# Optimization experiments

Hardware: AMD Instinct MI355X
Metric: run time of the kernel (lower is better)

## Reference

```python
import jax, jax.numpy as jnp
import numpy as np

D_MODEL = 1024
NHEAD = 8
HEAD_DIM = D_MODEL // NHEAD
D_FF = 4096
EPS_ATTN = 1e-6
EPS_LN = 1e-5


def _layernorm(x, g, b):
    mu = jnp.mean(x, axis=-1, keepdims=True)
    var = jnp.var(x, axis=-1, keepdims=True)
    return (x - mu) * jax.lax.rsqrt(var + EPS_LN) * g + b


def _linear_attention(q, k, v):
    # q,k,v: [N, L, H, D]
    Q = jax.nn.elu(q) + 1.0
    K = jax.nn.elu(k) + 1.0
    v_length = v.shape[1]
    v = v / v_length
    KV = jnp.einsum('nshd,nshv->nhdv', K, v)           # [N,H,D,D]
    Z = 1.0 / (jnp.einsum('nlhd,nhd->nlh', Q, K.sum(axis=1)) + EPS_ATTN)
    out = jnp.einsum('nlhd,nhdv,nlh->nlhv', Q, KV, Z) * v_length
    return out


def setup_inputs() -> dict:
    key = jax.random.key(0)
    ks = jax.random.split(key, 12)
    s = 1.0 / np.sqrt(D_MODEL)
    sf = 1.0 / np.sqrt(D_FF)
    return {
        'x': jax.random.normal(ks[0], (2, 4096, D_MODEL), jnp.float32),
        'wq': jax.random.normal(ks[1], (D_MODEL, D_MODEL), jnp.float32) * s,
        'wk': jax.random.normal(ks[2], (D_MODEL, D_MODEL), jnp.float32) * s,
        'wv': jax.random.normal(ks[3], (D_MODEL, D_MODEL), jnp.float32) * s,
        'w1': jax.random.normal(ks[4], (D_FF, D_MODEL), jnp.float32) * s,
        'b1': jnp.zeros((D_FF,), jnp.float32),
        'w2': jax.random.normal(ks[5], (D_MODEL, D_FF), jnp.float32) * sf,
        'b2': jnp.zeros((D_MODEL,), jnp.float32),
        'g1': jnp.ones((D_MODEL,), jnp.float32),
        'be1': jnp.zeros((D_MODEL,), jnp.float32),
        'g2': jnp.ones((D_MODEL,), jnp.float32),
        'be2': jnp.zeros((D_MODEL,), jnp.float32),
    }


def reference(x, wq, wk, wv, w1, b1, w2, b2, g1, be1, g2, be2):
    N, L, C = x.shape
    # pre-norm self attention
    x2 = _layernorm(x, g1, be1)
    q = (x2 @ wq.T).reshape(N, L, NHEAD, HEAD_DIM)
    k = (x2 @ wk.T).reshape(N, L, NHEAD, HEAD_DIM)
    v = (x2 @ wv.T).reshape(N, L, NHEAD, HEAD_DIM)
    msg = _linear_attention(q, k, v).reshape(N, L, C)
    x = x + msg
    # MLP block
    x2 = _layernorm(x, g2, be2)
    h = jax.nn.gelu(x2 @ w1.T + b1, approximate=False)
    x = x + (h @ w2.T + b2)
    return x
```

## Files before the change

### kernel.cpp

```cpp
#include <hip/hip_runtime.h>
#include <hip/hip_bf16.h>
#include <math.h>

typedef __bf16 bf16x8 __attribute__((ext_vector_type(8)));
typedef __bf16 bf16x4 __attribute__((ext_vector_type(4)));
typedef float f32x4 __attribute__((ext_vector_type(4)));

#define DEVI __device__ __forceinline__

DEVI void gload_lds16(const __bf16* g, __bf16* l) {
    __builtin_amdgcn_global_load_lds(
        (const __attribute__((address_space(1))) unsigned int*)g,
        (__attribute__((address_space(3))) unsigned int*)l, 16, 0, 0);
}

DEVI float fast_erf(float x) {
    const float ax = __builtin_fabsf(x);
    const float t = __builtin_amdgcn_rcpf(__builtin_fmaf(0.3275911f, ax, 1.0f));
    float p = __builtin_fmaf(1.061405429f, t, -1.453152027f);
    p = __builtin_fmaf(p, t, 1.421413741f);
    p = __builtin_fmaf(p, t, -0.284496736f);
    p = __builtin_fmaf(p, t, 0.254829592f);
    const float e = __expf(-ax * ax);
    const float r = __builtin_fmaf(-p * t, e, 1.0f);
    return __builtin_copysignf(r, x);
}

DEVI float gelu_exact(float v) {
    return 0.5f * v * (1.0f + fast_erf(v * 0.70710678118654752f));
}

DEVI int swz128(int row, int col) { return row * 128 + (col ^ ((row & 7) << 3)); }

__global__ void sniff_kernel(const unsigned short* __restrict__ x, int* flags) {
    const int tid = threadIdx.x;
    const unsigned short u = x[tid * 2];
    const int e = (u >> 7) & 0xFF;
    const int zero = (u == 0) ? 1 : 0;
    const int sane = ((e >= 0x71 && e <= 0x8E) || ((u & 0x7FFF) == 0)) ? 1 : 0;
    const unsigned long long mz = __ballot(zero != 0);
    const unsigned long long ms = __ballot(sane != 0);
    __shared__ int wz[4], wsn[4];
    if ((tid & 63) == 0) { wz[tid >> 6] = __popcll(mz); wsn[tid >> 6] = __popcll(ms); }
    __syncthreads();
    if (tid == 0) {
        const int nz = wz[0] + wz[1] + wz[2] + wz[3];
        const int ns = wsn[0] + wsn[1] + wsn[2] + wsn[3];
        flags[0] = (nz >= 192 || ns < 128) ? 1 : 0;
    }
}

DEVI void conv8(const void* src, __bf16* dst, int si, int di, int isf32) {
    if (isf32) {
        const float* s = (const float*)src + si;
        bf16x8 o;
#pragma unroll
        for (int j = 0; j < 8; j++) o[j] = (__bf16)s[j];
        *(bf16x8*)(dst + di) = o;
    } else {
        *(uint4*)(dst + di) = *(const uint4*)((const __bf16*)src + si);
    }
}

__global__ __launch_bounds__(256) void convert_kernel(const void* __restrict__ src,
                                                      __bf16* __restrict__ dst, int n,
                                                      const int* __restrict__ flags) {
    const int i = (blockIdx.x * 256 + threadIdx.x) * 8;
    if (i >= n) return;
    conv8(src, dst, i, i, flags[0]);
}

__global__ __launch_bounds__(256) void convert3_kernel(const void* s0, const void* s1,
                                                       const void* s2, __bf16* __restrict__ dst,
                                                       const int* __restrict__ flags) {
    const int i = (blockIdx.x * 256 + threadIdx.x) * 8;
    const int which = i >> 20;
    const int off = i & 1048575;
    const void* s = (which == 0) ? s0 : ((which == 1) ? s1 : s2);
    conv8(s, dst, off, i, flags[0]);
}

struct Ptr6 { const void* p[6]; };
__global__ __launch_bounds__(256) void convert_small(Ptr6 srcs, __bf16* __restrict__ d0,
                                                     __bf16* __restrict__ d1,
                                                     const int* __restrict__ flags) {
    const int idx = (blockIdx.x * 256 + threadIdx.x) * 8;
    if (idx >= 9216) return;
    const int f = flags[0];
    if (idx < 4096) {
        conv8(srcs.p[0], d0, idx, idx, f);
    } else {
        const int j = idx - 4096;
        conv8(srcs.p[1 + (j >> 10)], d1, j & 1023, j, f);
    }
}

__global__ __launch_bounds__(256) void convert_ln_kernel(
    const void* __restrict__ src, const __bf16* __restrict__ g,
    const __bf16* __restrict__ b, __bf16* __restrict__ cx,
    __bf16* __restrict__ x2, const int* __restrict__ flags) {
    const size_t row = blockIdx.x;
    const int tid = threadIdx.x;
    float v[4];
    if (flags[0]) {
        const float4 f = *((const float4*)((const float*)src + row * 1024) + tid);
        v[0] = f.x; v[1] = f.y; v[2] = f.z; v[3] = f.w;
    } else {
        const bf16x4 f = *((const bf16x4*)((const __bf16*)src + row * 1024) + tid);
#pragma unroll
        for (int i = 0; i < 4; i++) v[i] = (float)f[i];
    }
    bf16x4 o;
#pragma unroll
    for (int i = 0; i < 4; i++) o[i] = (__bf16)v[i];
    *((bf16x4*)(cx + row * 1024) + tid) = o;

    float s = v[0] + v[1] + v[2] + v[3];
    float s2 = v[0] * v[0] + v[1] * v[1] + v[2] * v[2] + v[3] * v[3];
#pragma unroll
    for (int m = 32; m >= 1; m >>= 1) {
        s += __shfl_xor(s, m, 64);
        s2 += __shfl_xor(s2, m, 64);
    }
    __shared__ float rs[4], rs2[4];
    const int wave = tid >> 6, lane = tid & 63;
    if (lane == 0) { rs[wave] = s; rs2[wave] = s2; }
    __syncthreads();
    s = rs[0] + rs[1] + rs[2] + rs[3];
    s2 = rs2[0] + rs2[1] + rs2[2] + rs2[3];
    const float mu = s * (1.0f / 1024.0f);
    const float var = s2 * (1.0f / 1024.0f) - mu * mu;
    const float inv = rsqrtf(var + 1e-5f);
#pragma unroll
    for (int i = 0; i < 4; i++) {
        const int c = tid * 4 + i;
        x2[row * 1024 + c] = (__bf16)((v[i] - mu) * inv * (float)g[c] + (float)b[c]);
    }
}

template <typename T>
__global__ __launch_bounds__(256) void ln_kernel(const T* __restrict__ x,
                                                 const __bf16* __restrict__ g,
                                                 const __bf16* __restrict__ b,
                                                 __bf16* __restrict__ out) {
    const size_t row = blockIdx.x;
    const T* xr = x + row * 1024;
    const int tid = threadIdx.x;
    float v[4];
#pragma unroll
    for (int i = 0; i < 4; i++) v[i] = (float)xr[tid * 4 + i];
    float s = v[0] + v[1] + v[2] + v[3];
    float s2 = v[0] * v[0] + v[1] * v[1] + v[2] * v[2] + v[3] * v[3];
#pragma unroll
    for (int m = 32; m >= 1; m >>= 1) {
        s += __shfl_xor(s, m, 64);
        s2 += __shfl_xor(s2, m, 64);
    }
    __shared__ float rs[4], rs2[4];
    const int wave = tid >> 6, lane = tid & 63;
    if (lane == 0) { rs[wave] = s; rs2[wave] = s2; }
    __syncthreads();
    s = rs[0] + rs[1] + rs[2] + rs[3];
    s2 = rs2[0] + rs2[1] + rs2[2] + rs2[3];
    const float mu = s * (1.0f / 1024.0f);
    const float var = s2 * (1.0f / 1024.0f) - mu * mu;
    const float inv = rsqrtf(var + 1e-5f);
#pragma unroll
    for (int i = 0; i < 4; i++) {
        const int c = tid * 4 + i;
        out[row * 1024 + c] = (__bf16)((v[i] - mu) * inv * (float)g[c] + (float)b[c]);
    }
}

enum { EP_NONE = 0, EP_ELU1 = 1, EP_BIAS_GELU = 2, EP_BIAS_RES = 3, EP_QKV = 4 };

template <int EP, typename OutT>
__global__ __launch_bounds__(256, 4) void gemm_bt(
    const __bf16* __restrict__ A, const __bf16* __restrict__ B,
    const __bf16* __restrict__ bias, const float* resid,
    OutT* C, int M, int N, int K) {
    const int nwg = gridDim.x * gridDim.y;
    int bid = blockIdx.y * gridDim.x + blockIdx.x;
    bid = (bid & 7) * (nwg >> 3) + (bid >> 3);
    const int bm = bid / gridDim.x, bn = bid % gridDim.x;

    const int tid = threadIdx.x;
    const int wave = tid >> 6, lane = tid & 63;
    const int wm = wave & 1, wn = wave >> 1;
    const int lm = lane & 15, lq = lane >> 4;

    __shared__ __align__(16) __bf16 Asmem[2][128 * 32];
    __shared__ __align__(16) __bf16 Bsmem[2][128 * 32];

    f32x4 acc[4][4] = {};

    const __bf16* Abase = A + (size_t)bm * 128 * K;
    const __bf16* Bbase = B + (size_t)bn * 128 * K;

    const int sr = tid >> 2;
    const int sc = (((tid & 3) ^ ((tid >> 3) & 3))) << 3;
    const int wb = wave * 512;

    const __bf16* Ap0 = Abase + (size_t)sr * K + sc;
    const __bf16* Ap1 = Abase + (size_t)(sr + 64) * K + sc;
    const __bf16* Bp0 = Bbase + (size_t)sr * K + sc;
    const __bf16* Bp1 = Bbase + (size_t)(sr + 64) * K + sc;

    const int rg = ((lq ^ ((lm >> 1) & 3))) << 3;

#define STAGE(b, kk)                              \
    do {                                          \
        gload_lds16(Ap0 + (kk), &Asmem[b][wb]);   \
        gload_lds16(Ap1 + (kk), &Asmem[b][2048 + wb]); \
        gload_lds16(Bp0 + (kk), &Bsmem[b][wb]);   \
        gload_lds16(Bp1 + (kk), &Bsmem[b][2048 + wb]); \
    } while (0)

    STAGE(0, 0);
    __syncthreads();
    int cur = 0;
    for (int k0 = 0; k0 < K; k0 += 32) {
        if (k0 + 32 < K) STAGE(cur ^ 1, k0 + 32);
        bf16x8 af[4], bfv[4];
#pragma unroll
        for (int i = 0; i < 4; i++) {
            af[i]  = *(const bf16x8*)&Asmem[cur][(wm * 64 + i * 16 + lm) * 32 + rg];
            bfv[i] = *(const bf16x8*)&Bsmem[cur][(wn * 64 + i * 16 + lm) * 32 + rg];
        }
#pragma unroll
        for (int i = 0; i < 4; i++)
#pragma unroll
            for (int j = 0; j < 4; j++)
                acc[i][j] = __builtin_amdgcn_mfma_f32_16x16x32_bf16(af[i], bfv[j], acc[i][j], 0, 0, 0);
        __syncthreads();
        cur ^= 1;
    }
#undef STAGE

    const int row0 = bm * 128 + wm * 64;
    const int col0 = bn * 128 + wn * 64;
#pragma unroll
    for (int i = 0; i < 4; i++) {
#pragma unroll
        for (int j = 0; j < 4; j++) {
            const int col = col0 + j * 16 + lm;
#pragma unroll
            for (int r = 0; r < 4; r++) {
                const int row = row0 + i * 16 + lq * 4 + r;
                float v = acc[i][j][r];
                if (EP == EP_QKV) {
                    const int which = col >> 10;
                    if (which < 2) v = (v > 0.0f) ? (v + 1.0f) : __expf(v);
                    ((__bf16*)C)[(size_t)which * 8388608 + (size_t)row * 1024 + (col & 1023)] = (__bf16)v;
                    continue;
                }
                if (EP == EP_ELU1) {
                    v = (v > 0.0f) ? (v + 1.0f) : __expf(v);
                } else if (EP == EP_BIAS_GELU) {
                    v += (float)bias[col];
                    v = gelu_exact(v);
                } else if (EP == EP_BIAS_RES) {
                    v += (float)bias[col];
                    v += resid[(size_t)row * N + col];
                }
                C[(size_t)row * N + col] = (OutT)v;
            }
        }
    }
}

__global__ __launch_bounds__(256, 2) void gemm_bt_k64(
    const __bf16* __restrict__ A, const __bf16* __restrict__ B,
    const __bf16* __restrict__ bias, const float* resid,
    float* C, int M, int N, int K) {
    const int nwg = gridDim.x * gridDim.y;
    int bid = blockIdx.y * gridDim.x + blockIdx.x;
    bid = (bid & 7) * (nwg >> 3) + (bid >> 3);
    const int bm = bid / gridDim.x, bn = bid % gridDim.x;

    const int tid = threadIdx.x;
    const int wave = tid >> 6, lane = tid & 63;
    const int wm = wave & 1, wn = wave >> 1;
    const int lm = lane & 15, lq = lane >> 4;

    __shared__ __align__(16) __bf16 Asmem[2][128 * 64];
    __shared__ __align__(16) __bf16 Bsmem[2][128 * 64];

    f32x4 acc[4][4] = {};

    const __bf16* Abase = A + (size_t)bm * 128 * K;
    const __bf16* Bbase = B + (size_t)bn * 128 * K;

    const int sr = tid >> 3;
    const int sc = (((tid & 7) ^ ((tid >> 3) & 7))) << 3;
    const int wb = wave * 512;

    const __bf16* Ap[4];
    const __bf16* Bp[4];
#pragma unroll
    for (int p = 0; p < 4; p++) {
        Ap[p] = Abase + (size_t)(p * 32 + sr) * K + sc;
        Bp[p] = Bbase + (size_t)(p * 32 + sr) * K + sc;
    }

#define STAGE64(b, kk)                                        \
    do {                                                      \
        _Pragma("unroll")                                     \
        for (int p = 0; p < 4; p++) {                         \
            gload_lds16(Ap[p] + (kk), &Asmem[b][p * 2048 + wb]); \
            gload_lds16(Bp[p] + (kk), &Bsmem[b][p * 2048 + wb]); \
        }                                                     \
    } while (0)

    STAGE64(0, 0);
    __syncthreads();
    int cur = 0;
    for (int k0 = 0; k0 < K; k0 += 64) {
        if (k0 + 64 < K) STAGE64(cur ^ 1, k0 + 64);
        bf16x8 af[2][4], bfv[2][4];
#pragma unroll
        for (int h = 0; h < 2; h++) {
            const int rg = ((h * 4 + lq) ^ (lm & 7)) << 3;
#pragma unroll
            for (int i = 0; i < 4; i++) {
                af[h][i]  = *(const bf16x8*)&Asmem[cur][(wm * 64 + i * 16 + lm) * 64 + rg];
                bfv[h][i] = *(const bf16x8*)&Bsmem[cur][(wn * 64 + i * 16 + lm) * 64 + rg];
            }
        }
#pragma unroll
        for (int h = 0; h < 2; h++)
#pragma unroll
            for (int i = 0; i < 4; i++)
#pragma unroll
                for (int j = 0; j < 4; j++)
                    acc[i][j] = __builtin_amdgcn_mfma_f32_16x16x32_bf16(af[h][i], bfv[h][j], acc[i][j], 0, 0, 0);
        __syncthreads();
        cur ^= 1;
    }
#undef STAGE64

    const int row0 = bm * 128 + wm * 64;
    const int col0 = bn * 128 + wn * 64;
#pragma unroll
    for (int i = 0; i < 4; i++) {
#pragma unroll
        for (int j = 0; j < 4; j++) {
            const int col = col0 + j * 16 + lm;
            const float bcol = (float)bias[col];
#pragma unroll
            for (int r = 0; r < 4; r++) {
                const int row = row0 + i * 16 + lq * 4 + r;
                float v = acc[i][j][r] + bcol;
                v += resid[(size_t)row * N + col];
                C[(size_t)row * N + col] = v;
            }
        }
    }
}

__global__ __launch_bounds__(256) void kv_kernel(const __bf16* __restrict__ Kf,
                                                 const __bf16* __restrict__ Vf,
                                                 float* __restrict__ pkv,
                                                 float* __restrict__ pks) {
    const int nh = blockIdx.x, sc = blockIdx.y, vh = blockIdx.z;
    const int n = nh >> 3, h = nh & 7;
    const int tid = threadIdx.x;
    const int tv = tid & 15, td = tid >> 4;
    __shared__ __align__(16) __bf16 Kt[32 * 128];
    __shared__ __align__(16) __bf16 Vt[32 * 64];
    float acc[8][4] = {};
    float ks[8] = {};
    const size_t rowbase = (size_t)n * 4096 + (size_t)sc * 256;
    for (int s0 = 0; s0 < 256; s0 += 32) {
#pragma unroll
        for (int rep = 0; rep < 2; rep++) {
            const int s = tid + rep * 256;
            const int r = s >> 4, cs = (s & 15) * 8;
            const size_t gidx = (rowbase + s0 + r) * 1024 + h * 128 + cs;
            *(bf16x8*)&Kt[r * 128 + cs] = *(const bf16x8*)&Kf[gidx];
        }
        {
            const int r = tid >> 3, cs = (tid & 7) * 8;
            const size_t gidx = (rowbase + s0 + r) * 1024 + h * 128 + vh * 64 + cs;
            *(bf16x8*)&Vt[r * 64 + cs] = *(const bf16x8*)&Vf[gidx];
        }
        __syncthreads();
#pragma unroll 4
        for (int s = 0; s < 32; s++) {
            const bf16x8 k8 = *(const bf16x8*)&Kt[s * 128 + td * 8];
            const bf16x4 v4 = *(const bf16x4*)&Vt[s * 64 + tv * 4];
            float kk[8], vv[4];
#pragma unroll
            for (int i = 0; i < 8; i++) kk[i] = (float)k8[i];
#pragma unroll
            for (int j = 0; j < 4; j++) vv[j] = (float)v4[j];
#pragma unroll
            for (int i = 0; i < 8; i++) {
                ks[i] += kk[i];
#pragma unroll
                for (int j = 0; j < 4; j++) acc[i][j] += kk[i] * vv[j];
            }
        }
        __syncthreads();
    }
    float* dst = pkv + ((size_t)sc * 16 + nh) * 16384;
#pragma unroll
    for (int j = 0; j < 4; j++)
#pragma unroll
        for (int i = 0; i < 8; i++)
            dst[(vh * 64 + tv * 4 + j) * 128 + td * 8 + i] = acc[i][j];
    if (vh == 0 && tv == 0) {
        float* ds2 = pks + ((size_t)sc * 16 + nh) * 128;
#pragma unroll
        for (int i = 0; i < 8; i++) ds2[td * 8 + i] = ks[i];
    }
}

__global__ __launch_bounds__(256) void kv_reduce(const float* __restrict__ pkv,
                                                 const float* __restrict__ pks,
                                                 __bf16* __restrict__ kvbT,
                                                 float* __restrict__ ksf) {
    const int idx = blockIdx.x * 256 + threadIdx.x;
    float s = 0.0f;
#pragma unroll
    for (int c = 0; c < 16; c++) s += pkv[(size_t)c * 262144 + idx];
    kvbT[idx] = (__bf16)s;
    if (idx < 2048) {
        float t = 0.0f;
#pragma unroll
        for (int c = 0; c < 16; c++) t += pks[c * 2048 + idx];
        ksf[idx] = t;
    }
}

__global__ __launch_bounds__(256) void z_kernel(const __bf16* __restrict__ Qf,
                                                const float* __restrict__ ksf,
                                                float* __restrict__ zbuf) {
    const int idx = blockIdx.x * 256 + threadIdx.x;
    const int h = idx & 7;
    const size_t row = (size_t)(idx >> 3);
    const __bf16* q = Qf + row * 1024 + h * 128;
    const float* ks = ksf + ((size_t)((row >> 12) * 8 + h)) * 128;
    float s = 0.0f;
    for (int d = 0; d < 128; d += 8) {
        const bf16x8 q8 = *(const bf16x8*)&q[d];
#pragma unroll
        for (int j = 0; j < 8; j++) s += (float)q8[j] * ks[d + j];
    }
    zbuf[idx] = 1.0f / (s + 1e-6f);
}

__global__ __launch_bounds__(256, 3) void attn_out_kernel(
    const __bf16* __restrict__ x, const __bf16* __restrict__ Qf,
    const __bf16* __restrict__ kvbT, const float* __restrict__ zbuf,
    float* __restrict__ xmid) {
    const int nh = blockIdx.x, lc = blockIdx.y;
    const int n = nh >> 3, h = nh & 7;
    const int tid = threadIdx.x;
    const int wv = tid >> 6, lane = tid & 63;
    const int lm = lane & 15, lq = lane >> 4;
    __shared__ __align__(16) __bf16 KVs[128 * 128];
    __shared__ __align__(16) __bf16 Qs[64 * 128];
    __shared__ float Zs[64];
    const __bf16* kv = kvbT + (size_t)nh * 16384;
#pragma unroll
    for (int rep = 0; rep < 8; rep++) {
        const int i = tid + rep * 256;
        const int r = i >> 4, c8 = (i & 15) * 8;
        *(bf16x8*)&KVs[swz128(r, c8)] = *(const bf16x8*)&kv[i * 8];
    }
    const size_t gr0 = (size_t)n * 4096 + (size_t)lc * 64;
#pragma unroll
    for (int rep = 0; rep < 4; rep++) {
        const int s = tid + rep * 256;
        const int r = s >> 4, cs = (s & 15) * 8;
        *(bf16x8*)&Qs[swz128(r, cs)] =
            *(const bf16x8*)&Qf[(gr0 + r) * 1024 + h * 128 + cs];
    }
    if (tid < 64) Zs[tid] = zbuf[(gr0 + tid) * 8 + h];
    __syncthreads();

    const int xmask = (lm & 7) << 3;
    f32x4 acc[4][2] = {};
#pragma unroll
    for (int k0 = 0; k0 < 128; k0 += 32) {
        const int kk = (k0 + lq * 8) ^ xmask;
        bf16x8 af[4], bv[2];
#pragma unroll
        for (int i = 0; i < 4; i++)
            af[i] = *(const bf16x8*)&Qs[(i * 16 + lm) * 128 + kk];
#pragma unroll
        for (int j = 0; j < 2; j++)
            bv[j] = *(const bf16x8*)&KVs[(wv * 32 + j * 16 + lm) * 128 + kk];
#pragma unroll
        for (int i = 0; i < 4; i++)
#pragma unroll
            for (int j = 0; j < 2; j++)
                acc[i][j] = __builtin_amdgcn_mfma_f32_16x16x32_bf16(af[i], bv[j], acc[i][j], 0, 0, 0);
    }
#pragma unroll
    for (int i = 0; i < 4; i++) {
#pragma unroll
        for (int j = 0; j < 2; j++) {
            const int col = wv * 32 + j * 16 + lm;
#pragma unroll
            for (int r = 0; r < 4; r++) {
                const int lr = i * 16 + lq * 4 + r;
                const size_t gi = (gr0 + lr) * 1024 + h * 128 + col;
                xmid[gi] = (float)x[gi] + acc[i][j][r] * Zs[lr];
            }
        }
    }
}

extern "C" void kernel_launch(void* const* d_in, const int* in_sizes, int n_in,
                              void* d_out, int out_size, void* d_ws, size_t ws_size,
                              hipStream_t stream) {
    float* out = (float*)d_out;
    char* ws = (char*)d_ws;

    const int nx = 8388608, nw = 1048576, nw1 = 4194304, nb1 = 4096, ng = 1024;
    size_t off = 0;
    __bf16* cx   = (__bf16*)(ws + off); off += (size_t)nx * 2;
    __bf16* cwq  = (__bf16*)(ws + off); off += (size_t)nw * 2;
    __bf16* cwk  = (__bf16*)(ws + off); off += (size_t)nw * 2;
    __bf16* cwv  = (__bf16*)(ws + off); off += (size_t)nw * 2;
    __bf16* cw1  = (__bf16*)(ws + off); off += (size_t)nw1 * 2;
    __bf16* cb1  = (__bf16*)(ws + off); off += (size_t)nb1 * 2;
    __bf16* cw2  = (__bf16*)(ws + off); off += (size_t)nw1 * 2;
    __bf16* cb2  = (__bf16*)(ws + off); off += (size_t)ng * 2;
    __bf16* cg1  = (__bf16*)(ws + off); off += (size_t)ng * 2;
    __bf16* cbe1 = (__bf16*)(ws + off); off += (size_t)ng * 2;
    __bf16* cg2  = (__bf16*)(ws + off); off += (size_t)ng * 2;
    __bf16* cbe2 = (__bf16*)(ws + off); off += (size_t)ng * 2;
    int* flags = (int*)(ws + off); off += 64;
    (void)cwk; (void)cwv; (void)cg1; (void)cbe1; (void)cg2; (void)cbe2;

    char* PB = ws + off;
    __bf16* x2   = (__bf16*)(PB);
    __bf16* Qf   = (__bf16*)(PB + 16777216);
    __bf16* Kf   = (__bf16*)(PB + 33554432);
    __bf16* Vf   = (__bf16*)(PB + 50331648);
    float*  pkv  = (float*)(PB + 67108864);
    float*  pks  = (float*)(PB + 83886080);
    float*  ksf  = (float*)(PB + 84017152);
    float*  zbuf = (float*)(PB + 84025344);
    __bf16* kvbT = (__bf16*)(PB + 84287488);
    __bf16* hbuf = (__bf16*)(PB + 16777216);
    float*  xmid = out;

    sniff_kernel<<<1, 256, 0, stream>>>((const unsigned short*)d_in[0], flags);
    convert3_kernel<<<3 * nw / 2048, 256, 0, stream>>>(d_in[1], d_in[2], d_in[3], cwq, flags);
    convert_kernel<<<nw1 / 2048, 256, 0, stream>>>(d_in[4], cw1, nw1, flags);
    convert_kernel<<<nw1 / 2048, 256, 0, stream>>>(d_in[6], cw2, nw1, flags);
    Ptr6 sp;
    sp.p[0] = d_in[5];  sp.p[1] = d_in[7];  sp.p[2] = d_in[8];
    sp.p[3] = d_in[9];  sp.p[4] = d_in[10]; sp.p[5] = d_in[11];
    convert_small<<<5, 256, 0, stream>>>(sp, cb1, cb2, flags);

    convert_ln_kernel<<<8192, 256, 0, stream>>>(d_in[0], cg1, cbe1, cx, x2, flags);
    gemm_bt<EP_QKV, __bf16><<<dim3(3072 / 128, 8192 / 128), 256, 0, stream>>>(
        x2, cwq, nullptr, nullptr, Qf, 8192, 3072, 1024);
    kv_kernel<<<dim3(16, 16, 2), 256, 0, stream>>>(Kf, Vf, pkv, pks);
    kv_reduce<<<1024, 256, 0, stream>>>(pkv, pks, kvbT, ksf);
    z_kernel<<<256, 256, 0, stream>>>(Qf, ksf, zbuf);
    attn_out_kernel<<<dim3(16, 64), 256, 0, stream>>>(cx, Qf, kvbT, zbuf, xmid);
    ln_kernel<float><<<8192, 256, 0, stream>>>(xmid, cg2, cbe2, x2);
    gemm_bt<EP_BIAS_GELU, __bf16><<<dim3(4096 / 128, 8192 / 128), 256, 0, stream>>>(
        x2, cw1, cb1, nullptr, hbuf, 8192, 4096, 1024);
    gemm_bt_k64<<<dim3(1024 / 128, 8192 / 128), 256, 0, stream>>>(
        hbuf, cw2, cb2, xmid, out, 8192, 1024, 4096);
}
```

Baseline: 463.1 us.

## Use 256x256-tile 512-thread GEMM kernel for the FFN up-projection with GELU

Adds a dedicated GEMM kernel for the first MLP projection that uses 256x256 output tiles, 8 waves, and a double-buffered LDS pipeline fed by direct global-to-LDS loads, with bias plus exact GELU in the epilogue. The larger tile raises arithmetic intensity and halves the number of global loads per FLOP compared with the 128x128 kernel. In exchange it uses 128 KB of LDS and a large accumulator array, which may limit occupancy to one block per CU despite launch_bounds(512,2). The grid shrinks to 512 workgroups, which can hurt wave-quantization balance across CUs.

```diff
diff --git a/kernel.cpp b/kernel.cpp
--- a/kernel.cpp
+++ b/kernel.cpp
@@ -269,6 +269,106 @@
     }
 }
 
+__global__ __launch_bounds__(512, 2) void gemm256_gelu(
+    const __bf16* __restrict__ A, const __bf16* __restrict__ B,
+    const __bf16* __restrict__ bias, __bf16* __restrict__ C,
+    int M, int N, int K) {
+    const int nwg = gridDim.x * gridDim.y;
+    int bid = blockIdx.y * gridDim.x + blockIdx.x;
+    bid = (bid & 7) * (nwg >> 3) + (bid >> 3);
+    const int bm = bid / gridDim.x, bn = bid % gridDim.x;
+
+    const int tid = threadIdx.x;
+    const int wave = tid >> 6, lane = tid & 63;
+    const int wm = wave >> 2, wn = wave & 3;
+    const int lm = lane & 15, lq = lane >> 4;
+
+    __shared__ __align__(16) __bf16 Asmem[2][256 * 64];
+    __shared__ __align__(16) __bf16 Bsmem[2][256 * 64];
+
+    f32x4 acc[8][4] = {};
+
+    const int sr = tid >> 3;
+    const int sc = (((tid & 7) ^ ((tid >> 3) & 7))) << 3;
+    const int wdst = wave * 512;
+
+    const __bf16* Ap[4];
+    const __bf16* Bp[4];
+#pragma unroll
+    for (int p = 0; p < 4; p++) {
+        Ap[p] = A + (size_t)(bm * 256 + p * 64 + sr) * K + sc;
+        Bp[p] = B + (size_t)(bn * 256 + p * 64 + sr) * K + sc;
+    }
+
+#define STAGE256(b, kk)                                          \
+    do {                                                         \
+        _Pragma("unroll")                                        \
+        for (int p = 0; p < 4; p++) {                            \
+            gload_lds16(Ap[p] + (kk), &Asmem[b][p * 4096 + wdst]); \
+            gload_lds16(Bp[p] + (kk), &Bsmem[b][p * 4096 + wdst]); \
+        }                                                        \
+    } while (0)
+
+    STAGE256(0, 0);
+    STAGE256(1, 64);
+    asm volatile("s_waitcnt vmcnt(8)" ::: "memory");
+    __builtin_amdgcn_s_barrier();
+    asm volatile("" ::: "memory");
+
+    const int gsw = lm & 7;
+    const int nt = K >> 6;
+    int cur = 0;
+    for (int t = 0; t < nt; ++t) {
+#pragma unroll
+        for (int ks = 0; ks < 2; ks++) {
+            const int rg = ((ks * 4 + lq) ^ gsw) << 3;
+            bf16x8 af[8], bv[4];
+#pragma unroll
+            for (int i = 0; i < 8; i++)
+                af[i] = *(const bf16x8*)&Asmem[cur][(wm * 128 + i * 16 + lm) * 64 + rg];
+#pragma unroll
+            for (int j = 0; j < 4; j++)
+                bv[j] = *(const bf16x8*)&Bsmem[cur][(wn * 64 + j * 16 + lm) * 64 + rg];
+            __builtin_amdgcn_s_setprio(1);
+#pragma unroll
+            for (int i = 0; i < 8; i++)
+#pragma unroll
+                for (int j = 0; j < 4; j++)
+                    acc[i][j] = __builtin_amdgcn_mfma_f32_16x16x32_bf16(af[i], bv[j], acc[i][j], 0, 0, 0);
+            __builtin_amdgcn_s_setprio(0);
+        }
+        asm volatile("" ::: "memory");
+        __builtin_amdgcn_s_barrier();
+        asm volatile("" ::: "memory");
+        if (t + 2 < nt) {
+            STAGE256(cur, (t + 2) << 6);
+            asm volatile("s_waitcnt vmcnt(8)" ::: "memory");
+        } else {
+            asm volatile("s_waitcnt vmcnt(0)" ::: "memory");
+        }
+        __builtin_amdgcn_s_barrier();
+        asm volatile("" ::: "memory");
+        cur ^= 1;
+    }
+#undef STAGE256
+
+    const int row0 = bm * 256 + wm * 128;
+    const int col0 = bn * 256 + wn * 64;
+#pragma unroll
+    for (int i = 0; i < 8; i++) {
+#pragma unroll
+        for (int j = 0; j < 4; j++) {
+            const int col = col0 + j * 16 + lm;
+            const float bcol = (float)bias[col];
+#pragma unroll
+            for (int r = 0; r < 4; r++) {
+                const int row = row0 + i * 16 + lq * 4 + r;
+                C[(size_t)row * N + col] = (__bf16)gelu_exact(acc[i][j][r] + bcol);
+            }
+        }
+    }
+}
+
 __global__ __launch_bounds__(256, 2) void gemm_bt_k64(
     const __bf16* __restrict__ A, const __bf16* __restrict__ B,
     const __bf16* __restrict__ bias, const float* resid,
@@ -566,8 +666,8 @@
     z_kernel<<<256, 256, 0, stream>>>(Qf, ksf, zbuf);
     attn_out_kernel<<<dim3(16, 64), 256, 0, stream>>>(cx, Qf, kvbT, zbuf, xmid);
     ln_kernel<float><<<8192, 256, 0, stream>>>(xmid, cg2, cbe2, x2);
-    gemm_bt<EP_BIAS_GELU, __bf16><<<dim3(4096 / 128, 8192 / 128), 256, 0, stream>>>(
-        x2, cw1, cb1, nullptr, hbuf, 8192, 4096, 1024);
+    gemm256_gelu<<<dim3(4096 / 256, 8192 / 256), 512, 0, stream>>>(
+        x2, cw1, cb1, hbuf, 8192, 4096, 1024);
     gemm_bt_k64<<<dim3(1024 / 128, 8192 / 128), 256, 0, stream>>>(
         hbuf, cw2, cb2, xmid, out, 8192, 1024, 4096);
 }
```

New measurement: 467.1 us. About the same (+0.9%).
